# Kernel tuning notes

Measured on AMD Instinct MI355X. Metric: run time of the kernel, lower is better.

The kernel has to match this reference:

```python
import jax, jax.numpy as jnp
import numpy as np


def setup_inputs() -> dict:
    key = jax.random.key(0)
    ks = jax.random.split(key, 10)
    B, L, H, E, D = 2, 2048, 16, 64, 64
    d_model = 512
    inp = {
        "queries": jax.random.normal(ks[0], (B, L, H, E), jnp.float32),
        "keys": jax.random.normal(ks[1], (B, L, H, E), jnp.float32),
        "values": jax.random.normal(ks[2], (B, L, H, D), jnp.float32),
        "raw_series": jax.random.normal(ks[3], (B, L, d_model), jnp.float32),
        # learned fusion MLP: Linear(d_model, d_model//2) -> ReLU -> Linear(d_model//2, 1)
        "w1": jax.random.normal(ks[4], (d_model, d_model // 2), jnp.float32) / np.sqrt(d_model),
        "b1": jnp.zeros((d_model // 2,), jnp.float32),
        "w2": jax.random.normal(ks[5], (d_model // 2, 1), jnp.float32) / np.sqrt(d_model // 2),
        "b2": jnp.zeros((1,), jnp.float32),
        # per-head trend scaling, init ones
        "alpha_trend": jnp.ones((H,), jnp.float32),
    }
    return inp


MOMENTUM_ALPHA = 1.0
MOMENTUM_K = 1


def reference(queries, keys, values, raw_series, w1, b1, w2, b2, alpha_trend):
    B, L, H, E = queries.shape
    scale = 1.0 / jnp.sqrt(jnp.asarray(E, queries.dtype))

    # ---- soft momentum bias ----
    # learned fusion: MLP over features -> scalar per position, [B, L]
    h = jax.nn.relu(raw_series @ w1 + b1)
    fused = (h @ w2 + b2)[..., 0]                       # [B, L]
    k = max(1, min(MOMENTUM_K, L - 1))
    momentum = fused[:, k:] - fused[:, :-k]              # [B, L-k]
    momentum = jnp.pad(momentum, ((0, 0), (k, 0)))       # left-pad zeros -> [B, L]
    diff = jnp.abs(momentum[:, :, None] - momentum[:, None, :])  # [B, L, L]
    soft_bias = -MOMENTUM_ALPHA * diff                   # [B, L, L]

    # ---- attention ----
    scores = jnp.einsum('blhe,bshe->bhls', queries, keys)  # [B, H, L, L]
    scores = scores + soft_bias[:, None, :, :] * alpha_trend[None, :, None, None]
    causal = jnp.triu(jnp.ones((L, L), bool), k=1)       # True above diagonal
    scores = jnp.where(causal[None, None], -jnp.inf, scores)
    A = jax.nn.softmax(scale * scores, axis=-1)          # [B, H, L, L]
    V = jnp.einsum('bhls,bshd->blhd', A, values)         # [B, L, H, D]
    return V
```

## Files before the change

kernel.cpp:

```cpp
#include <hip/hip_runtime.h>
#include <math.h>

#define B_ 2
#define L_ 2048
#define H_ 16
#define E_ 64
#define D_ 64
#define DM_ 512
#define DH_ 256

typedef __bf16 bf16_t;
typedef bf16_t bf16x8_t __attribute__((ext_vector_type(8)));
typedef float f32x4_t __attribute__((ext_vector_type(4)));

__device__ __forceinline__ unsigned bpack(float hi, float lo) {
    unsigned uh = __float_as_uint(hi) + 0x8000u;
    unsigned ul = __float_as_uint(lo) + 0x8000u;
    return __builtin_amdgcn_perm(uh, ul, 0x07060302u);
}

__device__ __forceinline__ bf16_t to_bf16(float f) {
    union { float f; unsigned u; } x; x.f = f;
    unsigned r = (x.u + 0x7fffu + ((x.u >> 16) & 1u)) >> 16;
    union { unsigned short s; bf16_t b; } y; y.s = (unsigned short)r;
    return y.b;
}

__global__ __launch_bounds__(256) void transpose_w1_kernel(
        const float* __restrict__ w1, bf16_t* __restrict__ w1t) {
    const int n = blockIdx.x;
    const int t = threadIdx.x;
    #pragma unroll
    for (int u = 0; u < 2; ++u) {
        int k = t + u * 256;
        float v = w1[(size_t)k * DH_ + n];
        w1t[(size_t)n * DM_ + k] = to_bf16(v);
    }
}

__global__ __launch_bounds__(512) void mlp_kernel(
        const float* __restrict__ raw, const bf16_t* __restrict__ w1t,
        const float* __restrict__ b1, const float* __restrict__ w2,
        const float* __restrict__ b2, float* __restrict__ fused) {
    __shared__ bf16_t Rs[16][520];
    __shared__ float pk[4][4][16][17];
    __shared__ float part[4][16];
    const int t = threadIdx.x;
    const int m0 = blockIdx.x * 16;
    #pragma unroll
    for (int u = 0; u < 4; ++u) {
        int idx = t + u * 512;
        int row = idx >> 7;
        int k = (idx & 127) << 2;
        f32x4_t v = *(const f32x4_t*)&raw[(size_t)(m0 + row) * DM_ + k];
        uint2 p;
        p.x = bpack(v[1], v[0]);
        p.y = bpack(v[3], v[2]);
        *(uint2*)&Rs[row][k] = p;
    }
    __syncthreads();
    const int wave = t >> 6;
    const int lane = t & 63;
    const int lrow = lane & 15;
    const int lgrp = lane >> 4;
    const int nq   = wave & 3;
    const int kh   = wave >> 2;
    const int n0w  = nq * 64;
    const int k0   = kh * 256;

    f32x4_t acc[4];
    #pragma unroll
    for (int nt = 0; nt < 4; ++nt) acc[nt] = (f32x4_t){0.f, 0.f, 0.f, 0.f};

    const bf16_t* wbase = w1t + (size_t)(n0w + lrow) * DM_ + k0 + lgrp * 8;
    #pragma unroll
    for (int s = 0; s < 8; ++s) {
        bf16x8_t a = *(const bf16x8_t*)&Rs[lrow][k0 + s * 32 + lgrp * 8];
        #pragma unroll
        for (int nt = 0; nt < 4; ++nt) {
            bf16x8_t b = *(const bf16x8_t*)(wbase + nt * 16 * DM_ + s * 32);
            acc[nt] = __builtin_amdgcn_mfma_f32_16x16x32_bf16(a, b, acc[nt], 0, 0, 0);
        }
    }
    if (kh == 1) {
        #pragma unroll
        for (int nt = 0; nt < 4; ++nt)
            #pragma unroll
            for (int r = 0; r < 4; ++r)
                pk[nq][nt][lgrp * 4 + r][lrow] = acc[nt][r];
    }
    __syncthreads();
    if (kh == 0) {
        float rowpart[4] = {0.f, 0.f, 0.f, 0.f};
        #pragma unroll
        for (int nt = 0; nt < 4; ++nt) {
            int n = n0w + nt * 16 + lrow;
            float b1v = b1[n];
            float w2v = w2[n];
            #pragma unroll
            for (int r = 0; r < 4; ++r) {
                float h = acc[nt][r] + pk[nq][nt][lgrp * 4 + r][lrow] + b1v;
                h = h > 0.f ? h : 0.f;
                rowpart[r] += h * w2v;
            }
        }
        #pragma unroll
        for (int r = 0; r < 4; ++r) {
            float v = rowpart[r];
            v += __shfl_xor(v, 1);
            v += __shfl_xor(v, 2);
            v += __shfl_xor(v, 4);
            v += __shfl_xor(v, 8);
            if (lrow == 0) part[nq][lgrp * 4 + r] = v;
        }
    }
    __syncthreads();
    if (t < 16)
        fused[m0 + t] = part[0][t] + part[1][t] + part[2][t] + part[3][t] + b2[0];
}

struct TileRegs { f32x4_t k[4]; float v[16]; float m; };

__global__ __launch_bounds__(256) void attn_kernel(
        const float* __restrict__ Q, const float* __restrict__ K,
        const float* __restrict__ V, const float* __restrict__ fused,
        const float* __restrict__ alpha_trend, float* __restrict__ out) {
    __shared__ bf16_t Ks[2][64][72];
    __shared__ bf16_t Vt[2][64][76];
    __shared__ unsigned short Ps[4][16][68];
    __shared__ float moms[2][64];

    const int bid  = blockIdx.x;
    const int bh   = bid & 31;
    const int qt   = 31 - (bid >> 5);
    const int h    = bh & 15;
    const int b    = bh >> 4;
    const int q0   = qt << 6;
    const int tid  = threadIdx.x;
    const int wave = tid >> 6;
    const int lane = tid & 63;
    const int lrow = lane & 15;
    const int lgrp = lane >> 4;

    const float c1      = 0.18033688f;
    const float ascale2 = alpha_trend[h] * c1;
    const size_t bl     = (size_t)b * L_;
    const int qw0       = q0 + wave * 16;

    const float* Kb = K + (bl * H_ + h) * E_;
    const float* Vb = V + (bl * H_ + h) * D_;
    const float* fp = fused + bl;

    const int krow = tid >> 4;
    const int ke0  = (tid & 15) << 2;
    const int vd   = tid & 63;
    const int vsb  = tid >> 6;

    bf16x8_t a_lo, a_hi;
    {
        const float* qp = Q + ((bl + qw0 + lrow) * H_ + h) * E_ + lgrp * 8;
        f32x4_t v0 = *(const f32x4_t*)(qp);
        f32x4_t v1 = *(const f32x4_t*)(qp + 4);
        f32x4_t v2 = *(const f32x4_t*)(qp + 32);
        f32x4_t v3 = *(const f32x4_t*)(qp + 36);
        #pragma unroll
        for (int k = 0; k < 4; ++k) {
            a_lo[k]     = to_bf16(v0[k] * c1);
            a_lo[4 + k] = to_bf16(v1[k] * c1);
            a_hi[k]     = to_bf16(v2[k] * c1);
            a_hi[4 + k] = to_bf16(v3[k] * c1);
        }
    }
    float mq[4];
    #pragma unroll
    for (int r = 0; r < 4; ++r) {
        int l = qw0 + lgrp * 4 + r;
        mq[r] = (l == 0) ? 0.f : fp[l] - fp[l - 1];
    }

    f32x4_t Oacc[4];
    #pragma unroll
    for (int c = 0; c < 4; ++c) Oacc[c] = (f32x4_t){0.f, 0.f, 0.f, 0.f};
    float rowsum[4] = {0.f, 0.f, 0.f, 0.f};

    TileRegs tr;
    #define LOAD_TILE(st_) do {                                                   \
        const int s0_ = (st_) << 6;                                               \
        _Pragma("unroll")                                                         \
        for (int u = 0; u < 4; ++u)                                               \
            tr.k[u] = *(const f32x4_t*)&Kb[(s0_ + krow + u * 16) * (H_ * E_) + ke0]; \
        _Pragma("unroll")                                                         \
        for (int j = 0; j < 16; ++j)                                              \
            tr.v[j] = Vb[(s0_ + vsb * 16 + j) * (H_ * D_) + vd];                  \
        if (tid < 64) {                                                           \
            int l_ = s0_ + tid;                                                   \
            tr.m = (l_ == 0) ? 0.f : fp[l_] - fp[l_ - 1];                         \
        }                                                                         \
    } while (0)

    #define STAGE_TILE(pb_) do {                                                  \
        _Pragma("unroll")                                                         \
        for (int u = 0; u < 4; ++u) {                                             \
            uint2 p;                                                              \
            p.x = bpack(tr.k[u][1], tr.k[u][0]);                                  \
            p.y = bpack(tr.k[u][3], tr.k[u][2]);                                  \
            *(uint2*)&Ks[pb_][krow + u * 16][ke0] = p;                            \
        }                                                                         \
        _Pragma("unroll")                                                         \
        for (int u = 0; u < 4; ++u) {                                             \
            uint2 p;                                                              \
            p.x = bpack(tr.v[u * 4 + 1], tr.v[u * 4 + 0]);                        \
            p.y = bpack(tr.v[u * 4 + 3], tr.v[u * 4 + 2]);                        \
            *(uint2*)&Vt[pb_][vd][vsb * 16 + u * 4] = p;                          \
        }                                                                         \
        if (tid < 64) moms[pb_][tid] = tr.m;                                      \
    } while (0)

    LOAD_TILE(0);
    STAGE_TILE(0);
    if (qt >= 1) LOAD_TILE(1);
    __syncthreads();

    for (int st = 0; st <= qt; ++st) {
        const int cb = st & 1;
        if (st < qt) STAGE_TILE((st + 1) & 1);
        if (st + 2 <= qt) LOAD_TILE(st + 2);

        f32x4_t Sacc[4];
        #pragma unroll
        for (int c = 0; c < 4; ++c) Sacc[c] = (f32x4_t){0.f, 0.f, 0.f, 0.f};
        #pragma unroll
        for (int c = 0; c < 4; ++c) {
            bf16x8_t b_lo = *(const bf16x8_t*)&Ks[cb][c * 16 + lrow][lgrp * 8];
            bf16x8_t b_hi = *(const bf16x8_t*)&Ks[cb][c * 16 + lrow][32 + lgrp * 8];
            Sacc[c] = __builtin_amdgcn_mfma_f32_16x16x32_bf16(a_lo, b_lo, Sacc[c], 0, 0, 0);
            Sacc[c] = __builtin_amdgcn_mfma_f32_16x16x32_bf16(a_hi, b_hi, Sacc[c], 0, 0, 0);
        }

        float rowe[4][4];
        #pragma unroll
        for (int c = 0; c < 4; ++c) {
            float ms = moms[cb][c * 16 + lrow];
            #pragma unroll
            for (int r = 0; r < 4; ++r) {
                float arg = Sacc[c][r] - ascale2 * fabsf(mq[r] - ms);
                rowe[c][r] = __builtin_amdgcn_exp2f(arg);
            }
        }
        if (st == qt) {
            const int s0 = st << 6;
            #pragma unroll
            for (int c = 0; c < 4; ++c) {
                int sg = s0 + c * 16 + lrow;
                #pragma unroll
                for (int r = 0; r < 4; ++r)
                    if (sg > qw0 + lgrp * 4 + r) rowe[c][r] = 0.f;
            }
        }
        unsigned short* Psw = &Ps[wave][0][0];
        #pragma unroll
        for (int c = 0; c < 4; ++c) {
            #pragma unroll
            for (int r = 0; r < 4; ++r) {
                unsigned u = (__float_as_uint(rowe[c][r]) + 0x8000u) & 0xffff0000u;
                Psw[(lgrp * 4 + r) * 68 + c * 16 + lrow] = (unsigned short)(u >> 16);
                rowsum[r] += __uint_as_float(u);
            }
        }

        #pragma unroll
        for (int hh = 0; hh < 2; ++hh) {
            union { uint2 u2[2]; bf16x8_t v; } ab;
            ab.u2[0] = *(const uint2*)&Psw[lrow * 68 + hh * 32 + lgrp * 8];
            ab.u2[1] = *(const uint2*)&Psw[lrow * 68 + hh * 32 + lgrp * 8 + 4];
            #pragma unroll
            for (int c2 = 0; c2 < 4; ++c2) {
                union { uint2 u2[2]; bf16x8_t v; } bb;
                bb.u2[0] = *(const uint2*)&Vt[cb][c2 * 16 + lrow][hh * 32 + lgrp * 8];
                bb.u2[1] = *(const uint2*)&Vt[cb][c2 * 16 + lrow][hh * 32 + lgrp * 8 + 4];
                Oacc[c2] = __builtin_amdgcn_mfma_f32_16x16x32_bf16(ab.v, bb.v, Oacc[c2], 0, 0, 0);
            }
        }
        __syncthreads();
    }

    #pragma unroll
    for (int r = 0; r < 4; ++r) {
        float rs = rowsum[r];
        rs += __shfl_xor(rs, 1);
        rs += __shfl_xor(rs, 2);
        rs += __shfl_xor(rs, 4);
        rs += __shfl_xor(rs, 8);
        float inv = 1.f / rs;
        size_t orow = ((bl + qw0 + lgrp * 4 + r) * H_ + h) * D_;
        #pragma unroll
        for (int c = 0; c < 4; ++c)
            out[orow + c * 16 + lrow] = Oacc[c][r] * inv;
    }
    #undef LOAD_TILE
    #undef STAGE_TILE
}

extern "C" void kernel_launch(void* const* d_in, const int* in_sizes, int n_in,
                              void* d_out, int out_size, void* d_ws, size_t ws_size,
                              hipStream_t stream) {
    const float* Q     = (const float*)d_in[0];
    const float* K     = (const float*)d_in[1];
    const float* V     = (const float*)d_in[2];
    const float* raw   = (const float*)d_in[3];
    const float* w1    = (const float*)d_in[4];
    const float* b1    = (const float*)d_in[5];
    const float* w2    = (const float*)d_in[6];
    const float* b2    = (const float*)d_in[7];
    const float* alpha = (const float*)d_in[8];
    float* out = (float*)d_out;

    float* fused = (float*)d_ws;
    bf16_t* w1t  = (bf16_t*)(fused + B_ * L_);

    transpose_w1_kernel<<<DH_, 256, 0, stream>>>(w1, w1t);
    mlp_kernel<<<B_ * L_ / 16, 512, 0, stream>>>(raw, w1t, b1, w2, b2, fused);
    attn_kernel<<<B_ * H_ * (L_ / 64), 256, 0, stream>>>(Q, K, V, fused, alpha, out);
}
```

Measured before the change: 170.9 us.

## Split long causal query tiles across two blocks and merge partial outputs

The upper half of the query tiles (the longest causal rows) is now split into two key-range chunks handled by separate blocks, giving 1536 blocks instead of 1024. Each chunk writes unnormalized bf16 partial outputs and row sums to workspace, and a new merge kernel adds them and normalizes. This works without a max-rescale because the softmax has no max subtraction. The aim is better load balance across the causal triangle. The K/V LDS staging also drops from double to single buffering, with a register prefetch and an extra barrier per tile, and the round-to-nearest on P is replaced by truncation. The costs are an extra launch, extra global traffic for the partials, and lower precision from storing the partial sums in bf16.

```diff
diff --git a/kernel.cpp b/kernel.cpp
--- a/kernel.cpp
+++ b/kernel.cpp
@@ -124,15 +124,30 @@
 __global__ __launch_bounds__(256) void attn_kernel(
         const float* __restrict__ Q, const float* __restrict__ K,
         const float* __restrict__ V, const float* __restrict__ fused,
-        const float* __restrict__ alpha_trend, float* __restrict__ out) {
-    __shared__ bf16_t Ks[2][64][72];
-    __shared__ bf16_t Vt[2][64][76];
+        const float* __restrict__ alpha_trend, float* __restrict__ out,
+        bf16_t* __restrict__ pO, float* __restrict__ prs) {
+    __shared__ bf16_t Ks[64][72];
+    __shared__ bf16_t Vt[64][70];
     __shared__ unsigned short Ps[4][16][68];
-    __shared__ float moms[2][64];
+    __shared__ float moms[64];
 
     const int bid  = blockIdx.x;
     const int bh   = bid & 31;
-    const int qt   = 31 - (bid >> 5);
+    const int wid  = bid >> 5;
+    int qt, sa, sb, chunk;
+    bool split;
+    if (wid < 32) {
+        qt    = 31 - (wid >> 1);
+        chunk = wid & 1;
+        int half = (qt + 2) >> 1;
+        sa = chunk ? half : 0;
+        sb = chunk ? qt + 1 : half;
+        split = true;
+    } else {
+        qt = 47 - wid;
+        sa = 0; sb = qt + 1; chunk = 0;
+        split = false;
+    }
     const int h    = bh & 15;
     const int b    = bh >> 4;
     const int q0   = qt << 6;
@@ -198,41 +213,35 @@
         }                                                                         \
     } while (0)
 
-    #define STAGE_TILE(pb_) do {                                                  \
-        _Pragma("unroll")                                                         \
-        for (int u = 0; u < 4; ++u) {                                             \
-            uint2 p;                                                              \
-            p.x = bpack(tr.k[u][1], tr.k[u][0]);                                  \
-            p.y = bpack(tr.k[u][3], tr.k[u][2]);                                  \
-            *(uint2*)&Ks[pb_][krow + u * 16][ke0] = p;                            \
-        }                                                                         \
-        _Pragma("unroll")                                                         \
-        for (int u = 0; u < 4; ++u) {                                             \
-            uint2 p;                                                              \
-            p.x = bpack(tr.v[u * 4 + 1], tr.v[u * 4 + 0]);                        \
-            p.y = bpack(tr.v[u * 4 + 3], tr.v[u * 4 + 2]);                        \
-            *(uint2*)&Vt[pb_][vd][vsb * 16 + u * 4] = p;                          \
-        }                                                                         \
-        if (tid < 64) moms[pb_][tid] = tr.m;                                      \
-    } while (0)
-
-    LOAD_TILE(0);
-    STAGE_TILE(0);
-    if (qt >= 1) LOAD_TILE(1);
-    __syncthreads();
-
-    for (int st = 0; st <= qt; ++st) {
-        const int cb = st & 1;
-        if (st < qt) STAGE_TILE((st + 1) & 1);
-        if (st + 2 <= qt) LOAD_TILE(st + 2);
+    LOAD_TILE(sa);
+
+    for (int st = sa; st < sb; ++st) {
+        __syncthreads();
+        #pragma unroll
+        for (int u = 0; u < 4; ++u) {
+            uint2 p;
+            p.x = bpack(tr.k[u][1], tr.k[u][0]);
+            p.y = bpack(tr.k[u][3], tr.k[u][2]);
+            *(uint2*)&Ks[krow + u * 16][ke0] = p;
+        }
+        #pragma unroll
+        for (int u = 0; u < 4; ++u) {
+            unsigned* vp = (unsigned*)&Vt[vd][vsb * 16 + u * 4];
+            vp[0] = bpack(tr.v[u * 4 + 1], tr.v[u * 4 + 0]);
+            vp[1] = bpack(tr.v[u * 4 + 3], tr.v[u * 4 + 2]);
+        }
+        if (tid < 64) moms[tid] = tr.m;
+        __syncthreads();
+
+        if (st + 1 < sb) LOAD_TILE(st + 1);
 
         f32x4_t Sacc[4];
         #pragma unroll
         for (int c = 0; c < 4; ++c) Sacc[c] = (f32x4_t){0.f, 0.f, 0.f, 0.f};
         #pragma unroll
         for (int c = 0; c < 4; ++c) {
-            bf16x8_t b_lo = *(const bf16x8_t*)&Ks[cb][c * 16 + lrow][lgrp * 8];
-            bf16x8_t b_hi = *(const bf16x8_t*)&Ks[cb][c * 16 + lrow][32 + lgrp * 8];
+            bf16x8_t b_lo = *(const bf16x8_t*)&Ks[c * 16 + lrow][lgrp * 8];
+            bf16x8_t b_hi = *(const bf16x8_t*)&Ks[c * 16 + lrow][32 + lgrp * 8];
             Sacc[c] = __builtin_amdgcn_mfma_f32_16x16x32_bf16(a_lo, b_lo, Sacc[c], 0, 0, 0);
             Sacc[c] = __builtin_amdgcn_mfma_f32_16x16x32_bf16(a_hi, b_hi, Sacc[c], 0, 0, 0);
         }
@@ -240,7 +249,7 @@
         float rowe[4][4];
         #pragma unroll
         for (int c = 0; c < 4; ++c) {
-            float ms = moms[cb][c * 16 + lrow];
+            float ms = moms[c * 16 + lrow];
             #pragma unroll
             for (int r = 0; r < 4; ++r) {
                 float arg = Sacc[c][r] - ascale2 * fabsf(mq[r] - ms);
@@ -262,9 +271,9 @@
         for (int c = 0; c < 4; ++c) {
             #pragma unroll
             for (int r = 0; r < 4; ++r) {
-                unsigned u = (__float_as_uint(rowe[c][r]) + 0x8000u) & 0xffff0000u;
-                Psw[(lgrp * 4 + r) * 68 + c * 16 + lrow] = (unsigned short)(u >> 16);
-                rowsum[r] += __uint_as_float(u);
+                Psw[(lgrp * 4 + r) * 68 + c * 16 + lrow] =
+                    (unsigned short)(__float_as_uint(rowe[c][r]) >> 16);
+                rowsum[r] += rowe[c][r];
             }
         }
 
@@ -275,30 +284,76 @@
             ab.u2[1] = *(const uint2*)&Psw[lrow * 68 + hh * 32 + lgrp * 8 + 4];
             #pragma unroll
             for (int c2 = 0; c2 < 4; ++c2) {
-                union { uint2 u2[2]; bf16x8_t v; } bb;
-                bb.u2[0] = *(const uint2*)&Vt[cb][c2 * 16 + lrow][hh * 32 + lgrp * 8];
-                bb.u2[1] = *(const uint2*)&Vt[cb][c2 * 16 + lrow][hh * 32 + lgrp * 8 + 4];
+                union { unsigned u[4]; bf16x8_t v; } bb;
+                const unsigned* vp = (const unsigned*)&Vt[c2 * 16 + lrow][hh * 32 + lgrp * 8];
+                bb.u[0] = vp[0]; bb.u[1] = vp[1]; bb.u[2] = vp[2]; bb.u[3] = vp[3];
                 Oacc[c2] = __builtin_amdgcn_mfma_f32_16x16x32_bf16(ab.v, bb.v, Oacc[c2], 0, 0, 0);
             }
         }
-        __syncthreads();
-    }
-
-    #pragma unroll
-    for (int r = 0; r < 4; ++r) {
-        float rs = rowsum[r];
-        rs += __shfl_xor(rs, 1);
-        rs += __shfl_xor(rs, 2);
-        rs += __shfl_xor(rs, 4);
-        rs += __shfl_xor(rs, 8);
-        float inv = 1.f / rs;
-        size_t orow = ((bl + qw0 + lgrp * 4 + r) * H_ + h) * D_;
-        #pragma unroll
-        for (int c = 0; c < 4; ++c)
-            out[orow + c * 16 + lrow] = Oacc[c][r] * inv;
+    }
+
+    if (!split) {
+        #pragma unroll
+        for (int r = 0; r < 4; ++r) {
+            float rs = rowsum[r];
+            rs += __shfl_xor(rs, 1);
+            rs += __shfl_xor(rs, 2);
+            rs += __shfl_xor(rs, 4);
+            rs += __shfl_xor(rs, 8);
+            float inv = 1.f / rs;
+            size_t orow = ((bl + qw0 + lgrp * 4 + r) * H_ + h) * D_;
+            #pragma unroll
+            for (int c = 0; c < 4; ++c)
+                out[orow + c * 16 + lrow] = Oacc[c][r] * inv;
+        }
+    } else {
+        const int slot = (bh * 16 + (qt - 16)) * 2 + chunk;
+        bf16_t* po = pO + (size_t)slot * 4096;
+        float*  pr = prs + (size_t)slot * 64;
+        #pragma unroll
+        for (int r = 0; r < 4; ++r) {
+            float rs = rowsum[r];
+            rs += __shfl_xor(rs, 1);
+            rs += __shfl_xor(rs, 2);
+            rs += __shfl_xor(rs, 4);
+            rs += __shfl_xor(rs, 8);
+            int q = wave * 16 + lgrp * 4 + r;
+            if (lrow == 0) pr[q] = rs;
+            #pragma unroll
+            for (int c = 0; c < 4; ++c)
+                po[q * 64 + c * 16 + lrow] = to_bf16(Oacc[c][r]);
+        }
     }
     #undef LOAD_TILE
-    #undef STAGE_TILE
+}
+
+__global__ __launch_bounds__(256) void merge_kernel(
+        const bf16_t* __restrict__ pO, const float* __restrict__ prs,
+        float* __restrict__ out) {
+    const int bid = blockIdx.x;
+    const int bh  = bid & 31;
+    const int qt  = 16 + (bid >> 5);
+    const int h   = bh & 15;
+    const int b   = bh >> 4;
+    const int t   = threadIdx.x;
+    const int q   = t >> 2;
+    const int d0  = (t & 3) << 4;
+
+    const int slotA = (bh * 16 + (qt - 16)) * 2;
+    const bf16_t* poA = pO + (size_t)slotA * 4096 + q * 64 + d0;
+    const bf16_t* poB = poA + 4096;
+    float rs = prs[slotA * 64 + q] + prs[(slotA + 1) * 64 + q];
+    float inv = 1.f / rs;
+
+    float* op = out + (((size_t)b * L_ + (qt << 6) + q) * H_ + h) * D_ + d0;
+    #pragma unroll
+    for (int i = 0; i < 16; i += 4) {
+        f32x4_t o;
+        #pragma unroll
+        for (int k = 0; k < 4; ++k)
+            o[k] = ((float)poA[i + k] + (float)poB[i + k]) * inv;
+        *(f32x4_t*)&op[i] = o;
+    }
 }
 
 extern "C" void kernel_launch(void* const* d_in, const int* in_sizes, int n_in,
@@ -317,8 +372,11 @@
 
     float* fused = (float*)d_ws;
     bf16_t* w1t  = (bf16_t*)(fused + B_ * L_);
+    bf16_t* pO   = w1t + (size_t)DH_ * DM_;
+    float* prs   = (float*)(pO + (size_t)1024 * 4096);
 
     transpose_w1_kernel<<<DH_, 256, 0, stream>>>(w1, w1t);
     mlp_kernel<<<B_ * L_ / 16, 512, 0, stream>>>(raw, w1t, b1, w2, b2, fused);
-    attn_kernel<<<B_ * H_ * (L_ / 64), 256, 0, stream>>>(Q, K, V, fused, alpha, out);
-}
+    attn_kernel<<<1536, 256, 0, stream>>>(Q, K, V, fused, alpha, out, pO, prs);
+    merge_kernel<<<512, 256, 0, stream>>>(pO, prs, out);
+}
```

Result: no change. 174.3 us (+2.0%).
